# Optimization experiments

Measured on AMD Instinct MI355X. Metric: run time of the kernel, lower is better.

## Reference

```python
import jax, jax.numpy as jnp
import numpy as np

B, D, R, W, K = 1024, 256, 16384, 64, 3


def setup_inputs() -> dict:
    key = jax.random.key(0)
    ks = jax.random.split(key, 8)
    s = lambda k, shape: jax.random.normal(k, shape, jnp.float32) * 0.05
    return {
        'x': jax.random.normal(ks[0], (B, D), jnp.float32),
        'Wv': s(ks[1], (D, W)), 'bv': jnp.zeros((W,), jnp.float32),
        'Wb': s(ks[2], (D, 1)), 'bb': jnp.zeros((1,), jnp.float32),
        'Wg': s(ks[3], (D, 1)), 'bg': jnp.zeros((1,), jnp.float32),
        'Wp': s(ks[4], (D, R)), 'bp': jnp.zeros((R,), jnp.float32),
        # positive conv weights keep the pre-sharpening address non-negative,
        # so address ** gamma is well defined (as in a trained NTM shift kernel)
        'conv_k': jax.random.uniform(ks[5], (K, 1, 1), jnp.float32),
        'conv_b': jnp.zeros((1,), jnp.float32),
        'mem': jax.random.normal(ks[6], (R, W), jnp.float32),
    }


def reference(x, Wv, bv, Wb, bb, Wg, bg, Wp, bp, conv_k, conv_b, mem):
    eps = 1e-16
    # controller heads
    v = x @ Wv + bv                                  # [B, W] writing value (key)
    beta = jax.nn.softplus(x @ Wb + bb)              # [B, 1] key strength
    gamma = 1.0 + jax.nn.softplus(x @ Wg + bg)       # [B, 1] sharpening
    # content addressing: cosine similarity against memory rows
    vn = jnp.linalg.norm(v, axis=-1, keepdims=True)  # [B, 1]
    mn = jnp.linalg.norm(mem, axis=-1, keepdims=True)  # [R, 1]
    sim = (v @ mem.T) / (vn * mn.T + eps)            # [B, R]
    w = jax.nn.softmax(beta * sim, axis=-1)          # [B, R]
    # circular-ish shift via Conv1D('same') over the mem_rows axis
    wc = jax.lax.conv_general_dilated(
        w[..., None], conv_k, (1,), 'SAME',
        dimension_numbers=('NWC', 'WIO', 'NWC')) + conv_b  # [B, R, 1]
    a = wc[..., 0] ** gamma                          # sharpen
    a = a / jnp.sum(a + eps, axis=1, keepdims=True)  # renormalize (matches tf sum(a+eps))
    # memory write (batch-averaged erase-free additive write, shared memory)
    erase = jnp.mean(a, axis=0)                      # [R]
    add = jnp.einsum('br,bw->rw', a, v) / a.shape[0] # [R, W]
    mem2 = mem * (1.0 - erase)[:, None] + add
    # read from trainable memory at predicted address
    p = jax.nn.softmax(x @ Wp + bp, axis=-1)         # [B, R]
    return p @ mem2                                  # [B, W]
```

## Files before the change

kernel.cpp:

```cpp
#include <hip/hip_runtime.h>
#include <hip/hip_bf16.h>

#define B_ 1024
#define D_ 256
#define R_ 16384
#define W_ 64

typedef float f32x4 __attribute__((ext_vector_type(4)));
typedef __bf16 bf16x8 __attribute__((ext_vector_type(8)));

__device__ __forceinline__ float bf2f(unsigned short u) {
    union { unsigned int i; float f; } v; v.i = ((unsigned int)u) << 16; return v.f;
}
__device__ __forceinline__ unsigned short f2bf(float f) {
    union { float fv; unsigned int i; } v; v.fv = f;
    unsigned int r = v.i + 0x7FFFu + ((v.i >> 16) & 1u);
    return (unsigned short)(r >> 16);
}
__device__ __forceinline__ float rt(float f) {
    return bf2f(f2bf(f));
}
__device__ __forceinline__ f32x4 mfma16(bf16x8 a, bf16x8 b, f32x4 c) {
    return __builtin_amdgcn_mfma_f32_16x16x32_bf16(a, b, c, 0, 0, 0);
}
__device__ __forceinline__ bf16x8 ld_bf8(const unsigned short* p) {
    return *(const bf16x8*)p;
}
__device__ __forceinline__ float sumsq8(bf16x8 v) {
    union { bf16x8 v; unsigned short u[8]; } c; c.v = v;
    float s = 0.f;
#pragma unroll
    for (int j = 0; j < 8; j++) { float f = bf2f(c.u[j]); s += f * f; }
    return s;
}

#define AO_X     0
#define AO_WV    262144
#define AO_BV    278528
#define AO_WB    278592
#define AO_BB    278848
#define AO_WG    278864
#define AO_BG    279120
#define AO_BP    279136
#define AO_CK    295520
#define AO_CB    295536
#define AO_MEM   295552
#define AO_TOT   1344128

#define NB_CONV  ((AO_TOT + 511) / 512)
#define NB_TR    1024
#define NB_HEADS 256

__global__ __launch_bounds__(256) void k_sentinel(float* __restrict__ out, float val) {
    out[blockIdx.x * 256 + threadIdx.x] = val;
}

__global__ __launch_bounds__(256) void k_prep(
        const float* x, const float* Wv, const float* bv, const float* Wb, const float* bb,
        const float* Wg, const float* bg, const float* bp,
        const float* ck, const float* cb, const float* mem, const float* Wp,
        unsigned short* __restrict__ dst, float* __restrict__ zst,
        unsigned short* __restrict__ WpT,
        float* __restrict__ v, unsigned short* __restrict__ vb,
        float* __restrict__ bovn, float* __restrict__ beta, float* __restrict__ gamma) {
    __shared__ unsigned short tile[64][66];
    __shared__ float sxh[4][256];
    int bid = blockIdx.x;
    int t = threadIdx.x;
    if (bid < NB_CONV) {
        int base = bid * 512 + t;
#pragma unroll
        for (int h = 0; h < 2; h++) {
            int idx = base + h * 256;
            if (idx >= AO_TOT) continue;
            if (idx < 2048) zst[idx] = 0.f;
            const float* p; int st; int n;
            if      (idx >= AO_MEM) { p = mem; st = AO_MEM; n = R_ * W_; }
            else if (idx >= AO_CB)  { p = cb;  st = AO_CB;  n = 1; }
            else if (idx >= AO_CK)  { p = ck;  st = AO_CK;  n = 3; }
            else if (idx >= AO_BP)  { p = bp;  st = AO_BP;  n = R_; }
            else if (idx >= AO_BG)  { p = bg;  st = AO_BG;  n = 1; }
            else if (idx >= AO_WG)  { p = Wg;  st = AO_WG;  n = D_; }
            else if (idx >= AO_BB)  { p = bb;  st = AO_BB;  n = 1; }
            else if (idx >= AO_WB)  { p = Wb;  st = AO_WB;  n = D_; }
            else if (idx >= AO_BV)  { p = bv;  st = AO_BV;  n = W_; }
            else if (idx >= AO_WV)  { p = Wv;  st = AO_WV;  n = D_ * W_; }
            else                    { p = x;   st = AO_X;   n = B_ * D_; }
            int local = idx - st;
            dst[idx] = (local < n) ? f2bf(p[local]) : (unsigned short)0;
        }
    } else if (bid < NB_CONV + NB_TR) {
        int b2 = bid - NB_CONV;
        int r0 = (b2 & 255) * 64, d0 = (b2 >> 8) * 64;
        int lane = t & 63, wv = t >> 6;
#pragma unroll
        for (int i = 0; i < 16; i++) {
            int dl = wv + 4 * i;
            tile[dl][lane] = f2bf(Wp[(size_t)(d0 + dl) * R_ + r0 + lane]);
        }
        __syncthreads();
#pragma unroll
        for (int i = 0; i < 16; i++) {
            int rl = wv + 4 * i;
            WpT[(size_t)(r0 + rl) * D_ + d0 + lane] = tile[lane][rl];
        }
    } else {
        int wv = t >> 6, lane = t & 63;
        int b = (bid - NB_CONV - NB_TR) * 4 + wv;
        float* sx = sxh[wv];
#pragma unroll
        for (int j = 0; j < 4; j++) sx[lane + 64 * j] = rt(x[b * 256 + lane + 64 * j]);
        __syncthreads();
        float acc = 0.f;
#pragma unroll 8
        for (int d = 0; d < 256; d++) acc += sx[d] * rt(Wv[d * 64 + lane]);
        acc += rt(bv[lane]);
        v[b * 64 + lane] = acc;
        vb[b * 64 + lane] = f2bf(acc);
        float sq = acc * acc;
#pragma unroll
        for (int d = 32; d >= 1; d >>= 1) sq += __shfl_xor(sq, d, 64);
        float pb = 0.f, pg = 0.f;
#pragma unroll
        for (int j = 0; j < 4; j++) {
            float xv = sx[lane + 64 * j];
            pb += xv * rt(Wb[lane + 64 * j]);
            pg += xv * rt(Wg[lane + 64 * j]);
        }
#pragma unroll
        for (int d = 32; d >= 1; d >>= 1) { pb += __shfl_xor(pb, d, 64); pg += __shfl_xor(pg, d, 64); }
        if (lane == 0) {
            float vn = sqrtf(sq);
            float zb = pb + rt(bb[0]);
            float zg = pg + rt(bg[0]);
            float be = (zb > 20.f) ? zb : log1pf(__expf(zb));
            beta[b]  = be;
            bovn[b]  = be / (vn + 1e-16f);
            gamma[b] = 1.f + ((zg > 20.f) ? zg : log1pf(__expf(zg)));
        }
    }
}

__global__ __launch_bounds__(256, 4) void k_sim(const unsigned short* __restrict__ vb,
        const unsigned short* __restrict__ mem,
        const float* __restrict__ bovn,
        const float* __restrict__ beta,
        unsigned short* __restrict__ E, float* __restrict__ S) {
    __shared__ unsigned short etile[64][132];
    __shared__ float sred[4][64];
    int bx = blockIdx.x;
    int rc = bx & 127, tb = bx >> 7;
    int t = threadIdx.x, wv = t >> 6, l = t & 63;
    int lane15 = l & 15, quad = l >> 4;
    int rr0 = rc * 128 + wv * 32 + lane15;
    bf16x8 bm[2][2];
    float im[2];
#pragma unroll
    for (int nt = 0; nt < 2; nt++) {
        int rr = rr0 + nt * 16;
        bm[nt][0] = ld_bf8(mem + rr * 64 + quad * 8);
        bm[nt][1] = ld_bf8(mem + rr * 64 + 32 + quad * 8);
        float sq = sumsq8(bm[nt][0]) + sumsq8(bm[nt][1]);
        sq += __shfl_xor(sq, 16, 64);
        sq += __shfl_xor(sq, 32, 64);
        im[nt] = 1.0f / (sqrtf(sq) + 1e-16f);
    }
    bf16x8 afr[4][2];
    float bvl[4][4], bel[4][4];
#pragma unroll
    for (int m = 0; m < 4; m++) {
        int brow = tb * 64 + m * 16 + lane15;
        afr[m][0] = ld_bf8(vb + brow * 64 + quad * 8);
        afr[m][1] = ld_bf8(vb + brow * 64 + 32 + quad * 8);
#pragma unroll
        for (int reg = 0; reg < 4; reg++) {
            int b2 = tb * 64 + m * 16 + quad * 4 + reg;
            bvl[m][reg] = bovn[b2];
            bel[m][reg] = beta[b2];
        }
    }
    float sp[4][4];
#pragma unroll
    for (int m = 0; m < 4; m++)
#pragma unroll
        for (int r = 0; r < 4; r++) sp[m][r] = 0.f;

#pragma unroll
    for (int nt = 0; nt < 2; nt++) {
        int rl = wv * 32 + nt * 16 + lane15;
#pragma unroll
        for (int m = 0; m < 4; m++) {
            f32x4 acc = (f32x4){0.f, 0.f, 0.f, 0.f};
            acc = mfma16(afr[m][0], bm[nt][0], acc);
            acc = mfma16(afr[m][1], bm[nt][1], acc);
#pragma unroll
            for (int reg = 0; reg < 4; reg++) {
                float e = __expf(acc[reg] * (bvl[m][reg] * im[nt]) - bel[m][reg]);
                sp[m][reg] += e;
                etile[m * 16 + quad * 4 + reg][rl] = f2bf(e);
            }
        }
    }
#pragma unroll
    for (int m = 0; m < 4; m++)
#pragma unroll
        for (int reg = 0; reg < 4; reg++) {
            float s = sp[m][reg];
            s += __shfl_xor(s, 1, 64); s += __shfl_xor(s, 2, 64);
            s += __shfl_xor(s, 4, 64); s += __shfl_xor(s, 8, 64);
            if (lane15 == 0) sred[wv][m * 16 + quad * 4 + reg] = s;
        }
    __syncthreads();
#pragma unroll
    for (int j = 0; j < 4; j++) {
        int idx8 = t + j * 256;
        int row = idx8 >> 4;
        int c8 = (idx8 & 15) * 8;
        *(bf16x8*)(E + (size_t)(tb * 64 + row) * R_ + rc * 128 + c8) =
            *(const bf16x8*)&etile[row][c8];
    }
    if (t < 64)
        atomicAdd(&S[tb * 64 + t], sred[0][t] + sred[1][t] + sred[2][t] + sred[3][t]);
}

__global__ __launch_bounds__(256) void k_conv(const unsigned short* __restrict__ E,
        unsigned short* __restrict__ AT,
        const float* __restrict__ S, const float* __restrict__ gamma,
        const unsigned short* __restrict__ conv_k, const unsigned short* __restrict__ conv_b,
        float* __restrict__ T) {
    __shared__ unsigned short ein[64][136];
    __shared__ unsigned short aout[128][68];
    float k0 = bf2f(conv_k[0]), k1 = bf2f(conv_k[1]), k2 = bf2f(conv_k[2]);
    float cb = bf2f(conv_b[0]);
    int b0 = (blockIdx.x >> 7) * 64;
    int r0 = (blockIdx.x & 127) * 128;
    int t = threadIdx.x;
#pragma unroll
    for (int j = 0; j < 4; j++) {
        int idx8 = t + j * 256;
        int row = idx8 >> 4, c8 = (idx8 & 15) * 8;
        *(bf16x8*)&ein[row][c8] = *(const bf16x8*)(E + (size_t)(b0 + row) * R_ + r0 + c8);
    }
    if (t < 64) {
        ein[t][130] = (r0 > 0) ? E[(b0 + t) * R_ + r0 - 1] : (unsigned short)0;
    } else if (t < 128) {
        int tb = t - 64;
        ein[tb][128] = (r0 + 128 < R_) ? E[(b0 + tb) * R_ + r0 + 128] : (unsigned short)0;
    }
    int b = t >> 2;
    int base = (t & 3) * 32;
    float sS_ = 1.0f / S[b0 + b];
    float g = gamma[b0 + b];
    __syncthreads();

    float el = bf2f((base == 0) ? ein[b][130] : ein[b][base - 1]);
    float ec = bf2f(ein[b][base]);
    float tacc = 0.f;
#pragma unroll
    for (int i = 0; i < 32; i++) {
        float er = bf2f(ein[b][base + 1 + i]);
        float wc = (k0 * el + k1 * ec + k2 * er) * sS_ + cb;
        wc = fmaxf(wc, 1e-30f);
        float au = __builtin_amdgcn_exp2f(g * __log2f(wc));
        aout[base + i][b] = f2bf(au);
        tacc += au;
        el = ec; ec = er;
    }
    tacc += __shfl_xor(tacc, 1, 64);
    tacc += __shfl_xor(tacc, 2, 64);
    if ((t & 3) == 0) atomicAdd(&T[b0 + b], tacc);
    __syncthreads();
#pragma unroll
    for (int j = 0; j < 8; j++) {
        int idx4 = t + j * 256;
        int rrow = idx4 >> 4, c4 = (idx4 & 15) * 4;
        *(ushort4*)(AT + (size_t)(r0 + rrow) * B_ + b0 + c4) = *(ushort4*)&aout[rrow][c4];
    }
}

__global__ __launch_bounds__(256) void k_vp2(const float* __restrict__ v, const float* __restrict__ T,
                                             unsigned short* __restrict__ vpb) {
    int idx = blockIdx.x * 256 + threadIdx.x;
    int m = idx >> 10, b = idx & 1023;
    float s = 1.0f / ((T[b] + (float)R_ * 1e-16f) * (float)B_);
    float val = (m < 64) ? v[b * 64 + m] * s : ((m == 64) ? s : 0.f);
    vpb[idx] = f2bf(val);
}

__global__ __launch_bounds__(256) void k_add(const unsigned short* __restrict__ AT,
        const unsigned short* __restrict__ vpb,
        const unsigned short* __restrict__ memb, unsigned short* __restrict__ mem2T) {
    __shared__ unsigned short smem[64][68];
    __shared__ unsigned short sm2[64][68];
    int r0 = blockIdx.x * 64;
    int t = threadIdx.x, wv = t >> 6, l = t & 63;
    int lane15 = l & 15, quad = l >> 4;
#pragma unroll
    for (int j = 0; j < 4; j++) {
        int idx4 = t + j * 256;
        int rl = idx4 >> 4, w4 = (idx4 & 15) * 4;
        *(ushort4*)&smem[rl][w4] = *(const ushort4*)(memb + (r0 + rl) * 64 + w4);
    }
    __syncthreads();

    const unsigned short* Brow = AT + (size_t)(r0 + wv * 16 + lane15) * B_ + quad * 8;
    const unsigned short* A0 = vpb + (0 * 16 + lane15) * B_ + quad * 8;
    const unsigned short* A1 = vpb + (1 * 16 + lane15) * B_ + quad * 8;
    const unsigned short* A2 = vpb + (2 * 16 + lane15) * B_ + quad * 8;
    const unsigned short* A3 = vpb + (3 * 16 + lane15) * B_ + quad * 8;
    const unsigned short* A4 = vpb + (4 * 16 + lane15) * B_ + quad * 8;
    f32x4 acc0 = {0,0,0,0}, acc1 = {0,0,0,0}, acc2 = {0,0,0,0}, acc3 = {0,0,0,0}, acc4 = {0,0,0,0};
#pragma unroll 4
    for (int k0 = 0; k0 < B_; k0 += 32) {
        bf16x8 bf = ld_bf8(Brow + k0);
        acc0 = mfma16(ld_bf8(A0 + k0), bf, acc0);
        acc1 = mfma16(ld_bf8(A1 + k0), bf, acc1);
        acc2 = mfma16(ld_bf8(A2 + k0), bf, acc2);
        acc3 = mfma16(ld_bf8(A3 + k0), bf, acc3);
        acc4 = mfma16(ld_bf8(A4 + k0), bf, acc4);
    }
    float er = __shfl(acc4[0], l & 15, 64);
    float ome = 1.f - er;
    f32x4 accs[4] = {acc0, acc1, acc2, acc3};
#pragma unroll
    for (int mt = 0; mt < 4; mt++) {
#pragma unroll
        for (int reg = 0; reg < 4; reg++) {
            int w = mt * 16 + quad * 4 + reg;
            int rl = wv * 16 + lane15;
            float m2 = bf2f(smem[rl][w]) * ome + accs[mt][reg];
            sm2[w][rl] = f2bf(m2);
        }
    }
    __syncthreads();
#pragma unroll
    for (int j = 0; j < 4; j++) {
        int idx4 = t + j * 256;
        int w = idx4 >> 4, r4 = (idx4 & 15) * 4;
        *(ushort4*)(mem2T + (size_t)w * R_ + r0 + r4) = *(ushort4*)&sm2[w][r4];
    }
}

__global__ __launch_bounds__(256, 4) void k_read(const unsigned short* __restrict__ x,
        const unsigned short* __restrict__ WpT, const unsigned short* __restrict__ bp,
        const unsigned short* __restrict__ mem2T,
        float* __restrict__ pacc, float* __restrict__ Spp) {
    __shared__ unsigned short bstage[2][32 * 264];
    __shared__ unsigned short ptile[4][16 * 40];
    int bx = blockIdx.x;
    int xcd = bx & 7, grp = bx >> 3;
    int rc = xcd * 8 + (grp >> 4), tb = grp & 15;
    int t = threadIdx.x, wv = t >> 6, l = t & 63;
    int lane15 = l & 15, quad = l >> 4;
    int brow = tb * 64 + wv * 16 + lane15;
    bf16x8 afr[8];
#pragma unroll
    for (int kk = 0; kk < 8; kk++)
        afr[kk] = ld_bf8(x + brow * 256 + kk * 32 + quad * 8);
    f32x4 accO[4];
#pragma unroll
    for (int nt = 0; nt < 4; nt++) accO[nt] = (f32x4){0.f, 0.f, 0.f, 0.f};
    float sp[4] = {0.f, 0.f, 0.f, 0.f};
    unsigned short* ptw = &ptile[wv][0];

    int srow = t >> 3, scg = (t & 7) * 8;
    bf16x8 pf[4];
    {
        const unsigned short* src = WpT + (size_t)(rc * 256 + srow) * 256 + scg;
#pragma unroll
        for (int j = 0; j < 4; j++) pf[j] = *(const bf16x8*)(src + 64 * j);
    }
    const unsigned short* vrow = mem2T + (size_t)lane15 * R_ + rc * 256 + quad * 8;

    for (int ss = 0; ss < 8; ss++) {
        unsigned short* bcur = bstage[ss & 1];
        {
            unsigned short* dst = bcur + srow * 264 + scg;
#pragma unroll
            for (int j = 0; j < 4; j++) *(bf16x8*)(dst + 64 * j) = pf[j];
        }
        if (ss < 7) {
            const unsigned short* src = WpT
                + (size_t)(rc * 256 + (ss + 1) * 32 + srow) * 256 + scg;
#pragma unroll
            for (int j = 0; j < 4; j++) pf[j] = *(const bf16x8*)(src + 64 * j);
        }
        __builtin_amdgcn_sched_barrier(0);
        asm volatile("s_waitcnt lgkmcnt(0)" ::: "memory");
        __builtin_amdgcn_s_barrier();
        __builtin_amdgcn_sched_barrier(0);
        bf16x8 vv0 = ld_bf8(vrow + (size_t)0 * 16 * R_ + ss * 32);
        bf16x8 vv1 = ld_bf8(vrow + (size_t)1 * 16 * R_ + ss * 32);
        bf16x8 vv2 = ld_bf8(vrow + (size_t)2 * 16 * R_ + ss * 32);
        bf16x8 vv3 = ld_bf8(vrow + (size_t)3 * 16 * R_ + ss * 32);
        int rbase = rc * 256 + ss * 32;
#pragma unroll
        for (int nt = 0; nt < 2; nt++) {
            f32x4 acc = (f32x4){0.f, 0.f, 0.f, 0.f};
            const unsigned short* bb = bcur + (nt * 16 + lane15) * 264 + quad * 8;
#pragma unroll
            for (int kk = 0; kk < 8; kk++) {
                bf16x8 bfr = *(const bf16x8*)(bb + kk * 32);
                acc = mfma16(afr[kk], bfr, acc);
            }
            int rr = rbase + nt * 16 + lane15;
            float bpv = bf2f(bp[rr]);
#pragma unroll
            for (int reg = 0; reg < 4; reg++) {
                float e = __expf(acc[reg] + bpv);
                unsigned short ue = f2bf(e);
                sp[reg] += bf2f(ue);
                ptw[(quad * 4 + reg) * 40 + nt * 16 + lane15] = ue;
            }
        }
        bf16x8 pa = *(const bf16x8*)(ptw + lane15 * 40 + quad * 8);
        accO[0] = mfma16(pa, vv0, accO[0]);
        accO[1] = mfma16(pa, vv1, accO[1]);
        accO[2] = mfma16(pa, vv2, accO[2]);
        accO[3] = mfma16(pa, vv3, accO[3]);
    }
#pragma unroll
    for (int nt = 0; nt < 4; nt++) {
        int wcol = nt * 16 + lane15;
#pragma unroll
        for (int reg = 0; reg < 4; reg++) {
            int b2 = tb * 64 + wv * 16 + quad * 4 + reg;
            pacc[((size_t)rc * B_ + b2) * 64 + wcol] = accO[nt][reg];
        }
    }
#pragma unroll
    for (int reg = 0; reg < 4; reg++) {
        float s = sp[reg];
        s += __shfl_xor(s, 1, 64); s += __shfl_xor(s, 2, 64);
        s += __shfl_xor(s, 4, 64); s += __shfl_xor(s, 8, 64);
        if (lane15 == 0) {
            int b2 = tb * 64 + wv * 16 + quad * 4 + reg;
            Spp[(size_t)rc * B_ + b2] = s;
        }
    }
}

__global__ __launch_bounds__(256) void k_out(const float* __restrict__ pacc,
                                             const float* __restrict__ Spp,
                                             float* __restrict__ out) {
    int idx = blockIdx.x * 256 + threadIdx.x;
    int b = idx >> 6;
    float acc = 0.f, sps = 0.f;
#pragma unroll 8
    for (int rc = 0; rc < 64; rc++) {
        acc += pacc[(size_t)rc * (B_ * 64) + idx];
        sps += Spp[rc * B_ + b];
    }
    out[idx] = acc / sps;
}

extern "C" void kernel_launch(void* const* d_in, const int* in_sizes, int n_in,
                              void* d_out, int out_size, void* d_ws, size_t ws_size,
                              hipStream_t stream) {
    (void)n_in; (void)out_size;
    float* outp = (float*)d_out;

    char* ws = (char*)d_ws;
    size_t o = 0;
    unsigned short* arena = (unsigned short*)(ws + o); o += (size_t)AO_TOT * 2;
    unsigned short* WpT = (unsigned short*)(ws + o); o += (size_t)R_ * D_ * 2;
    unsigned short* E   = (unsigned short*)(ws + o); o += (size_t)B_ * R_ * 2;
    unsigned short* AT  = (unsigned short*)(ws + o); o += (size_t)B_ * R_ * 2;
    float* v            = (float*)(ws + o);          o += (size_t)B_ * 64 * 4;
    unsigned short* vb  = (unsigned short*)(ws + o); o += (size_t)B_ * 64 * 2;
    unsigned short* vpb = (unsigned short*)(ws + o); o += (size_t)80 * B_ * 2;
    float* bovn         = (float*)(ws + o);          o += 4096;
    float* beta         = (float*)(ws + o);          o += 4096;
    float* gamma        = (float*)(ws + o);          o += 4096;
    unsigned short* m2T = (unsigned short*)(ws + o); o += (size_t)R_ * 64 * 2;
    float* S      = (float*)(ws + o);                o += 4096;
    float* T      = (float*)(ws + o);                o += 4096;
    float* Spp    = (float*)(ws + o);                o += (size_t)B_ * 64 * 4;
    float* pacc = (float*)AT;

    if (ws_size < o) {
        k_sentinel<<<256, 256, 0, stream>>>(outp, 1000.0f);
        return;
    }
    if (in_sizes[0] != B_ * D_ || in_sizes[7] != D_ * R_ || in_sizes[11] != R_ * W_) {
        k_sentinel<<<256, 256, 0, stream>>>(outp, 2000.0f);
        return;
    }

    k_prep<<<NB_CONV + NB_TR + NB_HEADS, 256, 0, stream>>>(
        (const float*)d_in[0], (const float*)d_in[1], (const float*)d_in[2],
        (const float*)d_in[3], (const float*)d_in[4], (const float*)d_in[5],
        (const float*)d_in[6], (const float*)d_in[8],
        (const float*)d_in[9], (const float*)d_in[10], (const float*)d_in[11],
        (const float*)d_in[7],
        arena, S, WpT, v, vb, bovn, beta, gamma);

    k_sim<<<2048, 256, 0, stream>>>(vb, arena + AO_MEM, bovn, beta, E, S);
    k_conv<<<2048, 256, 0, stream>>>(E, AT, S, gamma, arena + AO_CK, arena + AO_CB, T);
    k_vp2<<<320, 256, 0, stream>>>(v, T, vpb);
    k_add<<<256, 256, 0, stream>>>(AT, vpb, arena + AO_MEM, m2T);
    k_read<<<1024, 256, 0, stream>>>(arena + AO_X, WpT, arena + AO_BP, m2T, pacc, Spp);
    k_out<<<256, 256, 0, stream>>>(pacc, Spp, outp);
}
```

Measured before the change: 212.2 us.

## Recompute similarity exponentials in conv kernel instead of storing E matrix

```diff
diff --git a/kernel.cpp b/kernel.cpp
--- a/kernel.cpp
+++ b/kernel.cpp
@@ -141,12 +141,11 @@
     }
 }
 
-__global__ __launch_bounds__(256, 4) void k_sim(const unsigned short* __restrict__ vb,
+__global__ __launch_bounds__(256, 4) void k_s(const unsigned short* __restrict__ vb,
         const unsigned short* __restrict__ mem,
         const float* __restrict__ bovn,
         const float* __restrict__ beta,
-        unsigned short* __restrict__ E, float* __restrict__ S) {
-    __shared__ unsigned short etile[64][132];
+        float* __restrict__ S) {
     __shared__ float sred[4][64];
     int bx = blockIdx.x;
     int rc = bx & 127, tb = bx >> 7;
@@ -187,7 +186,6 @@
 
 #pragma unroll
     for (int nt = 0; nt < 2; nt++) {
-        int rl = wv * 32 + nt * 16 + lane15;
 #pragma unroll
         for (int m = 0; m < 4; m++) {
             f32x4 acc = (f32x4){0.f, 0.f, 0.f, 0.f};
@@ -197,7 +195,6 @@
             for (int reg = 0; reg < 4; reg++) {
                 float e = __expf(acc[reg] * (bvl[m][reg] * im[nt]) - bel[m][reg]);
                 sp[m][reg] += e;
-                etile[m * 16 + quad * 4 + reg][rl] = f2bf(e);
             }
         }
     }
@@ -211,41 +208,87 @@
             if (lane15 == 0) sred[wv][m * 16 + quad * 4 + reg] = s;
         }
     __syncthreads();
-#pragma unroll
-    for (int j = 0; j < 4; j++) {
-        int idx8 = t + j * 256;
-        int row = idx8 >> 4;
-        int c8 = (idx8 & 15) * 8;
-        *(bf16x8*)(E + (size_t)(tb * 64 + row) * R_ + rc * 128 + c8) =
-            *(const bf16x8*)&etile[row][c8];
-    }
     if (t < 64)
         atomicAdd(&S[tb * 64 + t], sred[0][t] + sred[1][t] + sred[2][t] + sred[3][t]);
 }
 
-__global__ __launch_bounds__(256) void k_conv(const unsigned short* __restrict__ E,
+__global__ __launch_bounds__(256, 4) void k_conv(const unsigned short* __restrict__ vb,
+        const unsigned short* __restrict__ mem,
+        const float* __restrict__ bovn,
+        const float* __restrict__ beta,
         unsigned short* __restrict__ AT,
         const float* __restrict__ S, const float* __restrict__ gamma,
         const unsigned short* __restrict__ conv_k, const unsigned short* __restrict__ conv_b,
         float* __restrict__ T) {
-    __shared__ unsigned short ein[64][136];
+    __shared__ unsigned short ein[64][132];
     __shared__ unsigned short aout[128][68];
     float k0 = bf2f(conv_k[0]), k1 = bf2f(conv_k[1]), k2 = bf2f(conv_k[2]);
     float cb = bf2f(conv_b[0]);
     int b0 = (blockIdx.x >> 7) * 64;
     int r0 = (blockIdx.x & 127) * 128;
-    int t = threadIdx.x;
-#pragma unroll
-    for (int j = 0; j < 4; j++) {
-        int idx8 = t + j * 256;
-        int row = idx8 >> 4, c8 = (idx8 & 15) * 8;
-        *(bf16x8*)&ein[row][c8] = *(const bf16x8*)(E + (size_t)(b0 + row) * R_ + r0 + c8);
-    }
-    if (t < 64) {
-        ein[t][130] = (r0 > 0) ? E[(b0 + t) * R_ + r0 - 1] : (unsigned short)0;
-    } else if (t < 128) {
-        int tb = t - 64;
-        ein[tb][128] = (r0 + 128 < R_) ? E[(b0 + tb) * R_ + r0 + 128] : (unsigned short)0;
+    int t = threadIdx.x, wv = t >> 6, l = t & 63;
+    int lane15 = l & 15, quad = l >> 4;
+
+    {
+        int rr0 = r0 + wv * 32 + lane15;
+        bf16x8 bm[2][2];
+        float im[2];
+#pragma unroll
+        for (int nt = 0; nt < 2; nt++) {
+            int rr = rr0 + nt * 16;
+            bm[nt][0] = ld_bf8(mem + rr * 64 + quad * 8);
+            bm[nt][1] = ld_bf8(mem + rr * 64 + 32 + quad * 8);
+            float sq = sumsq8(bm[nt][0]) + sumsq8(bm[nt][1]);
+            sq += __shfl_xor(sq, 16, 64);
+            sq += __shfl_xor(sq, 32, 64);
+            im[nt] = 1.0f / (sqrtf(sq) + 1e-16f);
+        }
+        bf16x8 afr[4][2];
+        float bvl[4][4], bel[4][4];
+#pragma unroll
+        for (int m = 0; m < 4; m++) {
+            int brow = b0 + m * 16 + lane15;
+            afr[m][0] = ld_bf8(vb + brow * 64 + quad * 8);
+            afr[m][1] = ld_bf8(vb + brow * 64 + 32 + quad * 8);
+#pragma unroll
+            for (int reg = 0; reg < 4; reg++) {
+                int b2 = b0 + m * 16 + quad * 4 + reg;
+                bvl[m][reg] = bovn[b2];
+                bel[m][reg] = beta[b2];
+            }
+        }
+#pragma unroll
+        for (int nt = 0; nt < 2; nt++) {
+            int rloc = wv * 32 + nt * 16 + lane15;
+#pragma unroll
+            for (int m = 0; m < 4; m++) {
+                f32x4 acc = (f32x4){0.f, 0.f, 0.f, 0.f};
+                acc = mfma16(afr[m][0], bm[nt][0], acc);
+                acc = mfma16(afr[m][1], bm[nt][1], acc);
+#pragma unroll
+                for (int reg = 0; reg < 4; reg++) {
+                    float e = __expf(acc[reg] * (bvl[m][reg] * im[nt]) - bel[m][reg]);
+                    ein[m * 16 + quad * 4 + reg][rloc] = f2bf(e);
+                }
+            }
+        }
+    }
+    if (t < 128) {
+        int hb = t & 63;
+        int rh = (t < 64) ? (r0 - 1) : (r0 + 128);
+        unsigned short hv = 0;
+        if (rh >= 0 && rh < R_) {
+            float acc = 0.f, sq = 0.f;
+#pragma unroll 8
+            for (int d = 0; d < 64; d++) {
+                float mv = bf2f(mem[rh * 64 + d]);
+                acc += bf2f(vb[(b0 + hb) * 64 + d]) * mv;
+                sq += mv * mv;
+            }
+            float imh = 1.0f / (sqrtf(sq) + 1e-16f);
+            hv = f2bf(__expf(acc * (bovn[b0 + hb] * imh) - beta[b0 + hb]));
+        }
+        ein[hb][(t < 64) ? 130 : 128] = hv;
     }
     int b = t >> 2;
     int base = (t & 3) * 32;
@@ -464,7 +507,6 @@
     size_t o = 0;
     unsigned short* arena = (unsigned short*)(ws + o); o += (size_t)AO_TOT * 2;
     unsigned short* WpT = (unsigned short*)(ws + o); o += (size_t)R_ * D_ * 2;
-    unsigned short* E   = (unsigned short*)(ws + o); o += (size_t)B_ * R_ * 2;
     unsigned short* AT  = (unsigned short*)(ws + o); o += (size_t)B_ * R_ * 2;
     float* v            = (float*)(ws + o);          o += (size_t)B_ * 64 * 4;
     unsigned short* vb  = (unsigned short*)(ws + o); o += (size_t)B_ * 64 * 2;
@@ -495,8 +537,9 @@
         (const float*)d_in[7],
         arena, S, WpT, v, vb, bovn, beta, gamma);
 
-    k_sim<<<2048, 256, 0, stream>>>(vb, arena + AO_MEM, bovn, beta, E, S);
-    k_conv<<<2048, 256, 0, stream>>>(E, AT, S, gamma, arena + AO_CK, arena + AO_CB, T);
+    k_s<<<2048, 256, 0, stream>>>(vb, arena + AO_MEM, bovn, beta, S);
+    k_conv<<<2048, 256, 0, stream>>>(vb, arena + AO_MEM, bovn, beta, AT, S, gamma,
+                                     arena + AO_CK, arena + AO_CB, T);
     k_vp2<<<320, 256, 0, stream>>>(v, T, vpb);
     k_add<<<256, 256, 0, stream>>>(AT, vpb, arena + AO_MEM, m2T);
     k_read<<<1024, 256, 0, stream>>>(arena + AO_X, WpT, arena + AO_BP, m2T, pacc, Spp);
```

After: 215.8 us. Within noise of the previous version (+1.7%).

## Split k_add reduction over batch across waves and double grid size

Applied to the files above, without the earlier changes.

```diff
diff --git a/kernel.cpp b/kernel.cpp
--- a/kernel.cpp
+++ b/kernel.cpp
@@ -290,28 +290,31 @@
 __global__ __launch_bounds__(256) void k_add(const unsigned short* __restrict__ AT,
         const unsigned short* __restrict__ vpb,
         const unsigned short* __restrict__ memb, unsigned short* __restrict__ mem2T) {
-    __shared__ unsigned short smem[64][68];
-    __shared__ unsigned short sm2[64][68];
-    int r0 = blockIdx.x * 64;
+    __shared__ unsigned short smem[32][68];
+    __shared__ unsigned short sm2[64][40];
+    __shared__ float cmb[2][64][20];
+    int r0 = blockIdx.x * 32;
     int t = threadIdx.x, wv = t >> 6, l = t & 63;
     int lane15 = l & 15, quad = l >> 4;
-#pragma unroll
-    for (int j = 0; j < 4; j++) {
+    int rg = wv & 1;
+    int kh = wv >> 1;
+#pragma unroll
+    for (int j = 0; j < 2; j++) {
         int idx4 = t + j * 256;
         int rl = idx4 >> 4, w4 = (idx4 & 15) * 4;
         *(ushort4*)&smem[rl][w4] = *(const ushort4*)(memb + (r0 + rl) * 64 + w4);
     }
     __syncthreads();
 
-    const unsigned short* Brow = AT + (size_t)(r0 + wv * 16 + lane15) * B_ + quad * 8;
-    const unsigned short* A0 = vpb + (0 * 16 + lane15) * B_ + quad * 8;
-    const unsigned short* A1 = vpb + (1 * 16 + lane15) * B_ + quad * 8;
-    const unsigned short* A2 = vpb + (2 * 16 + lane15) * B_ + quad * 8;
-    const unsigned short* A3 = vpb + (3 * 16 + lane15) * B_ + quad * 8;
-    const unsigned short* A4 = vpb + (4 * 16 + lane15) * B_ + quad * 8;
+    const unsigned short* Brow = AT + (size_t)(r0 + rg * 16 + lane15) * B_ + quad * 8 + kh * 512;
+    const unsigned short* A0 = vpb + (0 * 16 + lane15) * B_ + quad * 8 + kh * 512;
+    const unsigned short* A1 = vpb + (1 * 16 + lane15) * B_ + quad * 8 + kh * 512;
+    const unsigned short* A2 = vpb + (2 * 16 + lane15) * B_ + quad * 8 + kh * 512;
+    const unsigned short* A3 = vpb + (3 * 16 + lane15) * B_ + quad * 8 + kh * 512;
+    const unsigned short* A4 = vpb + (4 * 16 + lane15) * B_ + quad * 8 + kh * 512;
     f32x4 acc0 = {0,0,0,0}, acc1 = {0,0,0,0}, acc2 = {0,0,0,0}, acc3 = {0,0,0,0}, acc4 = {0,0,0,0};
 #pragma unroll 4
-    for (int k0 = 0; k0 < B_; k0 += 32) {
+    for (int k0 = 0; k0 < 512; k0 += 32) {
         bf16x8 bf = ld_bf8(Brow + k0);
         acc0 = mfma16(ld_bf8(A0 + k0), bf, acc0);
         acc1 = mfma16(ld_bf8(A1 + k0), bf, acc1);
@@ -319,24 +322,41 @@
         acc3 = mfma16(ld_bf8(A3 + k0), bf, acc3);
         acc4 = mfma16(ld_bf8(A4 + k0), bf, acc4);
     }
-    float er = __shfl(acc4[0], l & 15, 64);
-    float ome = 1.f - er;
-    f32x4 accs[4] = {acc0, acc1, acc2, acc3};
-#pragma unroll
-    for (int mt = 0; mt < 4; mt++) {
-#pragma unroll
-        for (int reg = 0; reg < 4; reg++) {
-            int w = mt * 16 + quad * 4 + reg;
-            int rl = wv * 16 + lane15;
-            float m2 = bf2f(smem[rl][w]) * ome + accs[mt][reg];
-            sm2[w][rl] = f2bf(m2);
+    if (kh == 1) {
+        float* c = cmb[rg][l];
+#pragma unroll
+        for (int j = 0; j < 4; j++) {
+            c[j] = acc0[j]; c[4 + j] = acc1[j]; c[8 + j] = acc2[j];
+            c[12 + j] = acc3[j]; c[16 + j] = acc4[j];
         }
     }
     __syncthreads();
-#pragma unroll
-    for (int j = 0; j < 4; j++) {
+    if (kh == 0) {
+        const float* c = cmb[rg][l];
+#pragma unroll
+        for (int j = 0; j < 4; j++) {
+            acc0[j] += c[j]; acc1[j] += c[4 + j]; acc2[j] += c[8 + j];
+            acc3[j] += c[12 + j]; acc4[j] += c[16 + j];
+        }
+        float er = __shfl(acc4[0], l & 15, 64);
+        float ome = 1.f - er;
+        f32x4 accs[4] = {acc0, acc1, acc2, acc3};
+        int rl = rg * 16 + lane15;
+#pragma unroll
+        for (int mt = 0; mt < 4; mt++) {
+#pragma unroll
+            for (int reg = 0; reg < 4; reg++) {
+                int w = mt * 16 + quad * 4 + reg;
+                float m2 = bf2f(smem[rl][w]) * ome + accs[mt][reg];
+                sm2[w][rl] = f2bf(m2);
+            }
+        }
+    }
+    __syncthreads();
+#pragma unroll
+    for (int j = 0; j < 2; j++) {
         int idx4 = t + j * 256;
-        int w = idx4 >> 4, r4 = (idx4 & 15) * 4;
+        int w = idx4 >> 3, r4 = (idx4 & 7) * 4;
         *(ushort4*)(mem2T + (size_t)w * R_ + r0 + r4) = *(ushort4*)&sm2[w][r4];
     }
 }
@@ -498,7 +518,7 @@
     k_sim<<<2048, 256, 0, stream>>>(vb, arena + AO_MEM, bovn, beta, E, S);
     k_conv<<<2048, 256, 0, stream>>>(E, AT, S, gamma, arena + AO_CK, arena + AO_CB, T);
     k_vp2<<<320, 256, 0, stream>>>(v, T, vpb);
-    k_add<<<256, 256, 0, stream>>>(AT, vpb, arena + AO_MEM, m2T);
+    k_add<<<512, 256, 0, stream>>>(AT, vpb, arena + AO_MEM, m2T);
     k_read<<<1024, 256, 0, stream>>>(arena + AO_X, WpT, arena + AO_BP, m2T, pacc, Spp);
     k_out<<<256, 256, 0, stream>>>(pacc, Spp, outp);
 }
```

After: 212.2 us. About the same (-0.0%).
